# Kernel tuning notes

Hardware: AMD Instinct MI355X
Metric: run time of the kernel (lower is better)

Reference implementation:

```python
import jax, jax.numpy as jnp
import numpy as np

# fp4 e2m1 representable magnitudes and round-to-nearest midpoints
_FP4_LEVELS = jnp.array([0.0, 0.5, 1.0, 1.5, 2.0, 3.0, 4.0, 6.0], dtype=jnp.float32)
_FP4_MIDS = jnp.array([0.25, 0.75, 1.25, 1.75, 2.5, 3.5, 5.0], dtype=jnp.float32)


def fp4_get_scalar(x):
    return jnp.mean(jnp.abs(x))


def fp4_quant_dequant(x, s):
    # quant(x, s) then rquant(x, s): round x/s to nearest fp4e2m1 value, scale back
    y = x / s
    idx = jnp.searchsorted(_FP4_MIDS, jnp.abs(y), side='right')
    q = jnp.sign(y) * _FP4_LEVELS[idx]
    return q * s


def setup_inputs() -> dict:
    key = jax.random.key(0)
    k1, k2, k3 = jax.random.split(key, 3)
    B, S, IN, OUT = 4, 2048, 4096, 4096
    input = jax.random.normal(k1, (B, S, IN), dtype=jnp.float32)
    # kaiming-uniform-ish weight, small bias
    bound_w = np.sqrt(6.0 / IN) / np.sqrt(1 + 5.0)
    weight = jax.random.uniform(k2, (OUT, IN), minval=-bound_w, maxval=bound_w, dtype=jnp.float32)
    bound_b = 1.0 / np.sqrt(IN)
    bias = jax.random.uniform(k3, (OUT,), minval=-bound_b, maxval=bound_b, dtype=jnp.float32)
    return {"input": input, "weight": weight, "bias": bias}


def reference(input, weight, bias):
    q_scalar = 1.0
    input_scalar = fp4_get_scalar(input) * q_scalar
    weight_scalar = fp4_get_scalar(weight) * q_scalar
    x_q = fp4_quant_dequant(input, input_scalar)      # [B,S,IN]
    w_q = fp4_quant_dequant(weight, weight_scalar)    # [OUT,IN]
    out = jnp.einsum('bsi,oi->bso', x_q, w_q) + bias  # [B,S,OUT]
    return out
```

## Files before the change

### kernel.cpp

```cpp
#include <hip/hip_runtime.h>
#include <hip/hip_bf16.h>
#include <stdint.h>

typedef __attribute__((ext_vector_type(16))) float f32x16;
typedef __attribute__((ext_vector_type(8))) int i32x8;

#define M_DIM 8192
#define N_DIM 4096
#define K_DIM 4096
#define NX_INV (1.0f / 33554432.0f)
#define NW_INV (1.0f / 16777216.0f)

__global__ void absum2_kernel(const float* __restrict__ x, const float* __restrict__ w,
                              double* __restrict__ sums) {
    bool isw = blockIdx.x >= 2048;
    const float4* src = (const float4*)(isw ? w : x);
    int n4  = isw ? (16777216 / 4) : (33554432 / 4);
    int bid = isw ? (blockIdx.x - 2048) : blockIdx.x;
    int nb  = isw ? 1024 : 2048;
    int i = bid * blockDim.x + threadIdx.x;
    int stride = nb * blockDim.x;
    float s = 0.f;
    for (; i < n4; i += stride) {
        float4 v = src[i];
        s += fabsf(v.x) + fabsf(v.y) + fabsf(v.z) + fabsf(v.w);
    }
    #pragma unroll
    for (int off = 32; off >= 1; off >>= 1) s += __shfl_down(s, off, 64);
    __shared__ float wsum[4];
    int lane = threadIdx.x & 63, wid = threadIdx.x >> 6;
    if (lane == 0) wsum[wid] = s;
    __syncthreads();
    if (threadIdx.x == 0) {
        double tot = (double)wsum[0] + (double)wsum[1] + (double)wsum[2] + (double)wsum[3];
        atomicAdd(&sums[isw ? 1 : 0], tot);
    }
}

__device__ __forceinline__ uint32_t enc_nib_t(float x, float t0, float t1, float t2,
                                              float t3, float t4, float t5, float t6) {
    float a = fabsf(x);
    uint32_t idx;
    if (a < t3) idx = (a < t1) ? ((a < t0) ? 0u : 1u) : ((a < t2) ? 2u : 3u);
    else        idx = (a < t5) ? ((a < t4) ? 4u : 5u) : ((a < t6) ? 6u : 7u);
    return idx | ((__float_as_uint(x) >> 31) << 3);
}

__global__ void quant2_kernel(const float* __restrict__ X, const float* __restrict__ W,
                              uint32_t* __restrict__ Xp, uint32_t* __restrict__ Wp,
                              const double* __restrict__ sums) {
    __shared__ float4 tile[32 * 64];

    bool isw = blockIdx.x >= 4096;
    const float* src_base = isw ? W : X;
    uint32_t* dst = isw ? Wp : Xp;
    float s = (float)(sums[isw ? 1 : 0]) * (isw ? NW_INV : NX_INV);
    int bid = isw ? (blockIdx.x - 4096) : blockIdx.x;

    float t0 = 0.25f * s, t1 = 0.75f * s, t2 = 1.25f * s, t3 = 1.75f * s;
    float t4 = 2.5f * s,  t5 = 3.5f * s,  t6 = 5.0f * s;

    int mb  = bid >> 4;
    int ktg = bid & 15;
    int t = threadIdx.x;

    {
        int row0 = t >> 6;
        int col4 = t & 63;
        const float4* src = (const float4*)(src_base + (size_t)(mb * 32 + row0) * K_DIM + ktg * 256) + col4;
        #pragma unroll
        for (int p = 0; p < 8; p++) {
            int row = p * 4 + row0;
            tile[row * 64 + (col4 ^ (row & 7))] = src[(size_t)p * 4 * (K_DIM / 4)];
        }
    }
    __syncthreads();

    int w = t >> 6;
    int l = t & 63;
    int row = l & 31;
    int ub = w * 16 + (l >> 5) * 8;
    uint32_t o[4];
    #pragma unroll
    for (int d = 0; d < 4; d++) {
        float4 f0 = tile[row * 64 + ((ub + 2 * d)     ^ (row & 7))];
        float4 f1 = tile[row * 64 + ((ub + 2 * d + 1) ^ (row & 7))];
        o[d] =  enc_nib_t(f0.x, t0,t1,t2,t3,t4,t5,t6)
             | (enc_nib_t(f0.y, t0,t1,t2,t3,t4,t5,t6) << 4)
             | (enc_nib_t(f0.z, t0,t1,t2,t3,t4,t5,t6) << 8)
             | (enc_nib_t(f0.w, t0,t1,t2,t3,t4,t5,t6) << 12)
             | (enc_nib_t(f1.x, t0,t1,t2,t3,t4,t5,t6) << 16)
             | (enc_nib_t(f1.y, t0,t1,t2,t3,t4,t5,t6) << 20)
             | (enc_nib_t(f1.z, t0,t1,t2,t3,t4,t5,t6) << 24)
             | (enc_nib_t(f1.w, t0,t1,t2,t3,t4,t5,t6) << 28);
    }
    int kt = ktg * 4 + w;
    *(uint4*)(dst + ((size_t)(mb * 64 + kt) * 64 + l) * 4) = make_uint4(o[0], o[1], o[2], o[3]);
}

#define NWG 512

__device__ __forceinline__ i32x8 dupfrag(uint4 u) {
    i32x8 v;
    v[0] = u.x; v[1] = u.y; v[2] = u.z; v[3] = u.w;
    v[4] = u.x; v[5] = u.y; v[6] = u.z; v[7] = u.w;
    return v;
}

#define LOADST(S, kt) do {                                      \
    S##a0 = *(const uint4*)(pA0 + (size_t)(kt) * 256);          \
    S##a1 = *(const uint4*)(pA1 + (size_t)(kt) * 256);          \
    S##a2 = *(const uint4*)(pA2 + (size_t)(kt) * 256);          \
    S##a3 = *(const uint4*)(pA3 + (size_t)(kt) * 256);          \
    S##b0 = *(const uint4*)(pB0 + (size_t)(kt) * 256);          \
    S##b1 = *(const uint4*)(pB1 + (size_t)(kt) * 256);          \
} while (0)

#define MFMA_ROW2(VA, B0, B1, C0, C1) do {                                        \
    i32x8 va_ = dupfrag(VA);                                                      \
    C0 = __builtin_amdgcn_mfma_scale_f32_32x32x64_f8f6f4(va_, B0, C0, 4, 4, 0, 0x7F7F7F7F, 0, 0x7F7F7F7F); \
    C1 = __builtin_amdgcn_mfma_scale_f32_32x32x64_f8f6f4(va_, B1, C1, 4, 4, 0, 0x7F7F7F7F, 0, 0x7F7F7F7F); \
} while (0)

#define MFMA_TILE(S) do {                                                         \
    i32x8 vb0_ = dupfrag(S##b0), vb1_ = dupfrag(S##b1);                           \
    __builtin_amdgcn_s_setprio(1);                                                \
    MFMA_ROW2(S##a0, vb0_, vb1_, acc00, acc01);                                   \
    MFMA_ROW2(S##a1, vb0_, vb1_, acc10, acc11);                                   \
    MFMA_ROW2(S##a2, vb0_, vb1_, acc20, acc21);                                   \
    MFMA_ROW2(S##a3, vb0_, vb1_, acc30, acc31);                                   \
    __builtin_amdgcn_s_setprio(0);                                                \
} while (0)

#define EPI(ACC, MM, NN) do {                                                     \
    int col_ = colb + (NN) * 32;                                                  \
    float bv_ = bias[col_];                                                       \
    _Pragma("unroll")                                                             \
    for (int i = 0; i < 16; i++) {                                                \
        int row_ = rowb + (MM) * 32 + (i & 3) + ((i >> 2) << 3);                  \
        __builtin_nontemporal_store(ACC[i] * scale + bv_,                         \
                                    &C[(size_t)row_ * N_DIM + col_]);             \
    }                                                                             \
} while (0)

__global__ __launch_bounds__(512, 2)
void gemm_kernel(const uint32_t* __restrict__ Ap, const uint32_t* __restrict__ Bp,
                 const float* __restrict__ bias, float* __restrict__ C,
                 const double* __restrict__ sums) {
    int bid = blockIdx.x;
    int swz = (bid & 7) * 64 + (bid >> 3);
    int bm = (swz >> 4) * 256;
    int bn = (swz & 15) * 256;

    int lane = threadIdx.x & 63;
    int wid = threadIdx.x >> 6;
    int wm = wid >> 2;
    int wn = wid & 3;

    const uint32_t* pA0 = Ap + (size_t)((bm >> 5) + wm * 4 + 0) * 16384 + lane * 4;
    const uint32_t* pA1 = Ap + (size_t)((bm >> 5) + wm * 4 + 1) * 16384 + lane * 4;
    const uint32_t* pA2 = Ap + (size_t)((bm >> 5) + wm * 4 + 2) * 16384 + lane * 4;
    const uint32_t* pA3 = Ap + (size_t)((bm >> 5) + wm * 4 + 3) * 16384 + lane * 4;
    const uint32_t* pB0 = Bp + (size_t)((bn >> 5) + wn * 2 + 0) * 16384 + lane * 4;
    const uint32_t* pB1 = Bp + (size_t)((bn >> 5) + wn * 2 + 1) * 16384 + lane * 4;

    f32x16 acc00 = (f32x16)0.f, acc01 = (f32x16)0.f;
    f32x16 acc10 = (f32x16)0.f, acc11 = (f32x16)0.f;
    f32x16 acc20 = (f32x16)0.f, acc21 = (f32x16)0.f;
    f32x16 acc30 = (f32x16)0.f, acc31 = (f32x16)0.f;

    uint4 S0a0, S0a1, S0a2, S0a3, S0b0, S0b1;
    uint4 S1a0, S1a1, S1a2, S1a3, S1b0, S1b1;

    LOADST(S0, 0);
    LOADST(S1, 1);
    for (int kt = 0; kt < 64; kt += 2) {
        MFMA_TILE(S0);
        if (kt + 2 < 64) LOADST(S0, kt + 2);
        MFMA_TILE(S1);
        if (kt + 3 < 64) LOADST(S1, kt + 3);
    }

    float scale = (float)((sums[0] * (1.0 / 33554432.0)) * (sums[1] * (1.0 / 16777216.0)));

    int colb = bn + wn * 64 + (lane & 31);
    int rowb = bm + wm * 128 + ((lane >> 5) << 2);
    EPI(acc00, 0, 0); EPI(acc01, 0, 1);
    EPI(acc10, 1, 0); EPI(acc11, 1, 1);
    EPI(acc20, 2, 0); EPI(acc21, 2, 1);
    EPI(acc30, 3, 0); EPI(acc31, 3, 1);
}

extern "C" void kernel_launch(void* const* d_in, const int* in_sizes, int n_in,
                              void* d_out, int out_size, void* d_ws, size_t ws_size,
                              hipStream_t stream) {
    const float* x    = (const float*)d_in[0];
    const float* w    = (const float*)d_in[1];
    const float* bias = (const float*)d_in[2];
    float* out = (float*)d_out;

    double* sums = (double*)d_ws;
    uint32_t* Xp = (uint32_t*)((char*)d_ws + 1024);
    uint32_t* Wp = Xp + (size_t)256 * 64 * 64 * 4;

    hipMemsetAsync(d_ws, 0, 1024, stream);
    absum2_kernel<<<3072, 256, 0, stream>>>(x, w, sums);
    quant2_kernel<<<6144, 256, 0, stream>>>(x, w, Xp, Wp, sums);
    gemm_kernel<<<NWG, 512, 0, stream>>>(Xp, Wp, bias, out, sums);
}
```

Baseline: 192.4 us.

## Stage GEMM operand tiles through LDS with async global_load_lds ring buffer

In the GEMM, per-wave direct global loads of A/B fragments are replaced by a cooperative block load. Each thread issues one 16-byte global_load_lds for A and one for B into a 4-slot LDS ring with a prefetch distance of two k-tiles. Waves then read their fragments from LDS and synchronise with s_waitcnt and barriers. The aim is to remove redundant global/L2 fetches, since each A tile was loaded by 4 waves and each B tile by 2, at the cost of 64KB LDS per block plus two barriers per k-step.

```diff
diff --git a/kernel.cpp b/kernel.cpp
--- a/kernel.cpp
+++ b/kernel.cpp
@@ -10,6 +10,9 @@
 #define K_DIM 4096
 #define NX_INV (1.0f / 33554432.0f)
 #define NW_INV (1.0f / 16777216.0f)
+
+#define AS3(p) ((__attribute__((address_space(3))) uint32_t*)(uint32_t)(uintptr_t)(p))
+#define AS1(p) ((const __attribute__((address_space(1))) uint32_t*)(uintptr_t)(p))
 
 __global__ void absum2_kernel(const float* __restrict__ x, const float* __restrict__ w,
                               double* __restrict__ sums) {
@@ -100,6 +103,10 @@
 
 #define NWG 512
 
+__device__ __forceinline__ void glds16(const uint32_t* g, uint32_t* l) {
+    __builtin_amdgcn_global_load_lds(AS1(g), AS3(l), 16, 0, 0);
+}
+
 __device__ __forceinline__ i32x8 dupfrag(uint4 u) {
     i32x8 v;
     v[0] = u.x; v[1] = u.y; v[2] = u.z; v[3] = u.w;
@@ -107,29 +114,10 @@
     return v;
 }
 
-#define LOADST(S, kt) do {                                      \
-    S##a0 = *(const uint4*)(pA0 + (size_t)(kt) * 256);          \
-    S##a1 = *(const uint4*)(pA1 + (size_t)(kt) * 256);          \
-    S##a2 = *(const uint4*)(pA2 + (size_t)(kt) * 256);          \
-    S##a3 = *(const uint4*)(pA3 + (size_t)(kt) * 256);          \
-    S##b0 = *(const uint4*)(pB0 + (size_t)(kt) * 256);          \
-    S##b1 = *(const uint4*)(pB1 + (size_t)(kt) * 256);          \
-} while (0)
-
-#define MFMA_ROW2(VA, B0, B1, C0, C1) do {                                        \
+#define MFMA2(VA, C0, C1) do {                                                    \
     i32x8 va_ = dupfrag(VA);                                                      \
-    C0 = __builtin_amdgcn_mfma_scale_f32_32x32x64_f8f6f4(va_, B0, C0, 4, 4, 0, 0x7F7F7F7F, 0, 0x7F7F7F7F); \
-    C1 = __builtin_amdgcn_mfma_scale_f32_32x32x64_f8f6f4(va_, B1, C1, 4, 4, 0, 0x7F7F7F7F, 0, 0x7F7F7F7F); \
-} while (0)
-
-#define MFMA_TILE(S) do {                                                         \
-    i32x8 vb0_ = dupfrag(S##b0), vb1_ = dupfrag(S##b1);                           \
-    __builtin_amdgcn_s_setprio(1);                                                \
-    MFMA_ROW2(S##a0, vb0_, vb1_, acc00, acc01);                                   \
-    MFMA_ROW2(S##a1, vb0_, vb1_, acc10, acc11);                                   \
-    MFMA_ROW2(S##a2, vb0_, vb1_, acc20, acc21);                                   \
-    MFMA_ROW2(S##a3, vb0_, vb1_, acc30, acc31);                                   \
-    __builtin_amdgcn_s_setprio(0);                                                \
+    C0 = __builtin_amdgcn_mfma_scale_f32_32x32x64_f8f6f4(va_, vb0_, C0, 4, 4, 0, 0x7F7F7F7F, 0, 0x7F7F7F7F); \
+    C1 = __builtin_amdgcn_mfma_scale_f32_32x32x64_f8f6f4(va_, vb1_, C1, 4, 4, 0, 0x7F7F7F7F, 0, 0x7F7F7F7F); \
 } while (0)
 
 #define EPI(ACC, MM, NN) do {                                                     \
@@ -147,38 +135,69 @@
 void gemm_kernel(const uint32_t* __restrict__ Ap, const uint32_t* __restrict__ Bp,
                  const float* __restrict__ bias, float* __restrict__ C,
                  const double* __restrict__ sums) {
+    __shared__ uint32_t lds[4 * 4096];
+
     int bid = blockIdx.x;
     int swz = (bid & 7) * 64 + (bid >> 3);
     int bm = (swz >> 4) * 256;
     int bn = (swz & 15) * 256;
 
-    int lane = threadIdx.x & 63;
-    int wid = threadIdx.x >> 6;
+    int t = threadIdx.x;
+    int lane = t & 63;
+    int wid = t >> 6;
     int wm = wid >> 2;
     int wn = wid & 3;
 
-    const uint32_t* pA0 = Ap + (size_t)((bm >> 5) + wm * 4 + 0) * 16384 + lane * 4;
-    const uint32_t* pA1 = Ap + (size_t)((bm >> 5) + wm * 4 + 1) * 16384 + lane * 4;
-    const uint32_t* pA2 = Ap + (size_t)((bm >> 5) + wm * 4 + 2) * 16384 + lane * 4;
-    const uint32_t* pA3 = Ap + (size_t)((bm >> 5) + wm * 4 + 3) * 16384 + lane * 4;
-    const uint32_t* pB0 = Bp + (size_t)((bn >> 5) + wn * 2 + 0) * 16384 + lane * 4;
-    const uint32_t* pB1 = Bp + (size_t)((bn >> 5) + wn * 2 + 1) * 16384 + lane * 4;
+    const uint32_t* gA = Ap + (size_t)((bm >> 5) + (t >> 6)) * 16384 + (t & 63) * 4;
+    const uint32_t* gB = Bp + (size_t)((bn >> 5) + (t >> 6)) * 16384 + (t & 63) * 4;
+    uint32_t* ldA = lds + t * 4;
+    uint32_t* ldB = lds + 2048 + t * 4;
+
+    int oA0 = ((wm * 4 + 0) * 64 + lane) * 4;
+    int oA1 = ((wm * 4 + 1) * 64 + lane) * 4;
+    int oA2 = ((wm * 4 + 2) * 64 + lane) * 4;
+    int oA3 = ((wm * 4 + 3) * 64 + lane) * 4;
+    int oB0 = 2048 + ((wn * 2 + 0) * 64 + lane) * 4;
+    int oB1 = 2048 + ((wn * 2 + 1) * 64 + lane) * 4;
 
     f32x16 acc00 = (f32x16)0.f, acc01 = (f32x16)0.f;
     f32x16 acc10 = (f32x16)0.f, acc11 = (f32x16)0.f;
     f32x16 acc20 = (f32x16)0.f, acc21 = (f32x16)0.f;
     f32x16 acc30 = (f32x16)0.f, acc31 = (f32x16)0.f;
 
-    uint4 S0a0, S0a1, S0a2, S0a3, S0b0, S0b1;
-    uint4 S1a0, S1a1, S1a2, S1a3, S1b0, S1b1;
-
-    LOADST(S0, 0);
-    LOADST(S1, 1);
-    for (int kt = 0; kt < 64; kt += 2) {
-        MFMA_TILE(S0);
-        if (kt + 2 < 64) LOADST(S0, kt + 2);
-        MFMA_TILE(S1);
-        if (kt + 3 < 64) LOADST(S1, kt + 3);
+    glds16(gA + 0,   ldA + 0);
+    glds16(gB + 0,   ldB + 0);
+    glds16(gA + 256, ldA + 4096);
+    glds16(gB + 256, ldB + 4096);
+
+    for (int kt = 0; kt < 64; kt++) {
+        if (kt < 63) asm volatile("s_waitcnt vmcnt(2)" ::: "memory");
+        else         asm volatile("s_waitcnt vmcnt(0)" ::: "memory");
+        __builtin_amdgcn_s_barrier();
+
+        const uint32_t* rb = lds + (kt & 3) * 4096;
+        int so = ((kt + 2) & 3) * 4096;
+
+        if (kt < 62) glds16(gA + (kt + 2) * 256, ldA + so);
+        uint4 rA0 = *(const uint4*)&rb[oA0];
+        uint4 rA1 = *(const uint4*)&rb[oA1];
+        uint4 rB0 = *(const uint4*)&rb[oB0];
+        uint4 rB1 = *(const uint4*)&rb[oB1];
+        i32x8 vb0_ = dupfrag(rB0);
+        i32x8 vb1_ = dupfrag(rB1);
+        __builtin_amdgcn_s_setprio(1);
+        MFMA2(rA0, acc00, acc01);
+        MFMA2(rA1, acc10, acc11);
+        __builtin_amdgcn_s_setprio(0);
+        __builtin_amdgcn_s_barrier();
+
+        if (kt < 62) glds16(gB + (kt + 2) * 256, ldB + so);
+        uint4 rA2 = *(const uint4*)&rb[oA2];
+        uint4 rA3 = *(const uint4*)&rb[oA3];
+        __builtin_amdgcn_s_setprio(1);
+        MFMA2(rA2, acc20, acc21);
+        MFMA2(rA3, acc30, acc31);
+        __builtin_amdgcn_s_setprio(0);
     }
 
     float scale = (float)((sums[0] * (1.0 / 33554432.0)) * (sums[1] * (1.0 / 16777216.0)));
```

Measured after the change: 220.3 us. 1.14x slower.
